# Kernel optimization log

Hardware: AMD Instinct MI355X
Metric: run time of the kernel (lower is better)

Reference implementation:

```python
import jax, jax.numpy as jnp
import numpy as np

D_MODEL = 1024
NUM_HEADS = 16
D_KEY = 64
CTX = 2048
B, T = 2, 2048


def setup_inputs() -> dict:
    key = jax.random.key(0)
    ks = jax.random.split(key, 5)
    scale_in = 1.0 / np.sqrt(D_MODEL)
    scale_out = 1.0 / np.sqrt(NUM_HEADS * D_KEY)
    return {
        "X": jax.random.normal(ks[0], (B, T, D_MODEL), dtype=jnp.float32),
        "Wqkv": jax.random.uniform(ks[1], (D_MODEL, 3 * NUM_HEADS * D_KEY), dtype=jnp.float32, minval=-scale_in, maxval=scale_in),
        "bqkv": jax.random.uniform(ks[2], (3 * NUM_HEADS * D_KEY,), dtype=jnp.float32, minval=-scale_in, maxval=scale_in),
        "Wout": jax.random.uniform(ks[3], (NUM_HEADS * D_KEY, D_MODEL), dtype=jnp.float32, minval=-scale_out, maxval=scale_out),
        "bout": jax.random.uniform(ks[4], (D_MODEL,), dtype=jnp.float32, minval=-scale_out, maxval=scale_out),
    }


def reference(X, Wqkv, bqkv, Wout, bout):
    b, t, _ = X.shape
    # project and split into q, k, v: [B,T,3,H,Dk]
    qkv = (X @ Wqkv + bqkv).reshape(b, t, 3, NUM_HEADS, D_KEY)
    q = qkv[:, :, 0].transpose(0, 2, 1, 3)  # [B,H,T,Dk]
    k = qkv[:, :, 1].transpose(0, 2, 1, 3)
    v = qkv[:, :, 2].transpose(0, 2, 1, 3)
    scores = jnp.einsum("bhqd,bhkd->bhqk", q, k) / jnp.sqrt(jnp.float32(D_KEY))
    causal = jnp.tril(jnp.ones((t, t), dtype=bool))  # [T,T]
    scores = jnp.where(causal, scores, -jnp.inf)
    attn = jax.nn.softmax(scores, axis=-1)
    out = jnp.einsum("bhqk,bhkd->bhqd", attn, v)  # [B,H,T,Dk]
    out = out.transpose(0, 2, 1, 3).reshape(b, t, NUM_HEADS * D_KEY)
    return out @ Wout + bout
```

## Files before the change

### kernel.cpp

```cpp
#include <hip/hip_runtime.h>
#include <hip/hip_bf16.h>
#include <math.h>

static constexpr int Bc = 2, Hc = 16, Tc = 2048, DKc = 64, DMc = 1024, NQKV = 3072;
#define QSCALE 0.18033688011112042f

typedef unsigned short u16;
typedef unsigned int u32;
typedef short s8v __attribute__((ext_vector_type(8)));
typedef float f32x4 __attribute__((ext_vector_type(4)));
typedef float f32x16 __attribute__((ext_vector_type(16)));
typedef int i32x4 __attribute__((ext_vector_type(4)));

#define DEVINL __device__ __forceinline__

DEVINL u16 f2b(float f) {
    union { float f; unsigned u; } v; v.f = f;
    unsigned u = v.u;
    unsigned r = (u + 0x7fffu + ((u >> 16) & 1u)) >> 16;
    return (u16)r;
}

DEVINL u32 pkbf16(float lo, float up) {
    u32 r;
    asm volatile("v_cvt_pk_bf16_f32 %0, %1, %2" : "=v"(r) : "v"(lo), "v"(up));
    return r;
}

DEVINL float vexp2(float x) {
    float r;
    asm("v_exp_f32 %0, %1" : "=v"(r) : "v"(x));
    return r;
}

DEVINL void pl32swap(u32& a, u32& b) {
    asm volatile("v_permlane32_swap_b32 %0, %1" : "+v"(a), "+v"(b));
}

DEVINL void gl_lds(const void* g, void* l) {
    __builtin_amdgcn_global_load_lds(
        (const __attribute__((address_space(1))) unsigned int*)g,
        (__attribute__((address_space(3))) unsigned int*)l, 16, 0, 0);
}

DEVINL s8v as_s8v(i32x4 x) { union { i32x4 i; s8v v; } u; u.i = x; return u.v; }

DEVINL void transw_tile(const float* __restrict__ W, u16* __restrict__ Wt,
                        int N, int K, int n0, int k0, u16 (*LT)[72], int t) {
    const int rr = t >> 4, cc = (t & 15) * 4;
    #pragma unroll
    for (int it = 0; it < 4; it++) {
        const int row = it * 16 + rr;
        float4 f = *(const float4*)&W[(size_t)(k0 + row) * N + n0 + cc];
        union { u16 u[4]; uint2 d; } o;
        o.u[0] = f2b(f.x); o.u[1] = f2b(f.y); o.u[2] = f2b(f.z); o.u[3] = f2b(f.w);
        *(uint2*)&LT[row][cc] = o.d;
    }
    __syncthreads();
    #pragma unroll
    for (int it = 0; it < 4; it++) {
        const int nrow = it * 16 + rr;
        union { u16 u[4]; uint2 d; } o;
        #pragma unroll
        for (int j = 0; j < 4; j++) o.u[j] = LT[cc + j][nrow];
        *(uint2*)&Wt[(size_t)(n0 + nrow) * K + k0 + cc] = o.d;
    }
}

__global__ __launch_bounds__(256) void prepass(
    const float* __restrict__ X, u16* __restrict__ Xb,
    const float* __restrict__ Wqkv, u16* __restrict__ Wt1,
    const float* __restrict__ Wout, u16* __restrict__ Wt2)
{
    __shared__ u16 LT[64][72];
    const int bid = blockIdx.x, t = threadIdx.x;
    if (bid < 1024) {
        const int n4 = (Bc * Tc * DMc) / 4;
        for (int i = bid * 256 + t; i < n4; i += 1024 * 256) {
            float4 f = ((const float4*)X)[i];
            union { u16 u[4]; uint2 d; } o;
            o.u[0] = f2b(f.x); o.u[1] = f2b(f.y); o.u[2] = f2b(f.z); o.u[3] = f2b(f.w);
            ((uint2*)Xb)[i] = o.d;
        }
    } else if (bid < 1024 + 768) {
        const int b2 = bid - 1024;
        transw_tile(Wqkv, Wt1, NQKV, DMc, (b2 % 48) * 64, (b2 / 48) * 64, LT, t);
    } else {
        const int b2 = bid - 1792;
        transw_tile(Wout, Wt2, DMc, DMc, (b2 % 16) * 64, (b2 / 16) * 64, LT, t);
    }
}

template <int EPI>
__global__ __launch_bounds__(512) void gemm_cv(
    const u16* __restrict__ A, const u16* __restrict__ Bt,
    const float* __restrict__ bias,
    u16* __restrict__ q_out, u16* __restrict__ k_out, u16* __restrict__ v_out,
    float* __restrict__ f_out, int M, int N, int K, int ntn)
{
    __shared__ __align__(16) u16 Al[2][128 * 32];
    __shared__ __align__(16) u16 Bl[2][128 * 32];
    const int tid = threadIdx.x, lane = tid & 63, w = tid >> 6;
    const int qd = gridDim.x >> 3;
    const int wg = (blockIdx.x & 7) * qd + (blockIdx.x >> 3);
    const int m0 = (wg / ntn) * 128, n0 = (wg % ntn) * 128;
    const int wm = w >> 2, wn = w & 3;

    f32x4 acc[4][2] = {};
    const int nt = K >> 5;

    const int srow = tid >> 2;
    const int skc  = ((tid & 3) ^ ((srow >> 1) & 3)) * 8;

#define STG(t_, s_) do {                                                       \
        const int kk_ = (t_) << 5;                                             \
        gl_lds(A + (size_t)(m0 + srow) * K + kk_ + skc,                        \
               (char*)&Al[s_][0] + w * 1024);                                  \
        gl_lds(Bt + (size_t)(n0 + srow) * K + kk_ + skc,                       \
               (char*)&Bl[s_][0] + w * 1024);                                  \
    } while (0)
#define BARX() do { __builtin_amdgcn_sched_barrier(0);                         \
        __builtin_amdgcn_s_barrier();                                          \
        __builtin_amdgcn_sched_barrier(0); } while (0)

    STG(0, 0);
    int buf = 0;
    for (int t = 0; t < nt; t++) {
        if (t + 1 < nt) {
            STG(t + 1, buf ^ 1);
            asm volatile("s_waitcnt vmcnt(2)" ::: "memory");
        } else {
            asm volatile("s_waitcnt vmcnt(0)" ::: "memory");
        }
        BARX();
        s8v af[4], bf[2];
        #pragma unroll
        for (int mi = 0; mi < 4; mi++) {
            const int row = wm * 64 + mi * 16 + (lane & 15);
            const int slot = (lane >> 4) ^ ((row >> 1) & 3);
            af[mi] = *(const s8v*)((const char*)&Al[buf][0] + row * 64 + slot * 16);
        }
        #pragma unroll
        for (int ni = 0; ni < 2; ni++) {
            const int row = wn * 32 + ni * 16 + (lane & 15);
            const int slot = (lane >> 4) ^ ((row >> 1) & 3);
            bf[ni] = *(const s8v*)((const char*)&Bl[buf][0] + row * 64 + slot * 16);
        }
        #pragma unroll
        for (int mi = 0; mi < 4; mi++)
            #pragma unroll
            for (int ni = 0; ni < 2; ni++)
                acc[mi][ni] = __builtin_amdgcn_mfma_f32_16x16x32_bf16(af[mi], bf[ni], acc[mi][ni], 0, 0, 0);
        BARX();
        buf ^= 1;
    }
#undef STG
#undef BARX

    #pragma unroll
    for (int mi = 0; mi < 4; mi++)
    #pragma unroll
    for (int ni = 0; ni < 2; ni++)
    #pragma unroll
    for (int r = 0; r < 4; r++) {
        const int row = m0 + wm * 64 + mi * 16 + (lane >> 4) * 4 + r;
        const int col = n0 + wn * 32 + ni * 16 + (lane & 15);
        const float val = acc[mi][ni][r] + bias[col];
        if constexpr (EPI == 0) {
            const int sel = col >> 10, rem = col & 1023;
            const int h = rem >> 6, d = rem & 63;
            const int b = row >> 11, tt = row & 2047;
            const size_t idx = ((size_t)(b * Hc + h) * Tc + tt) * DKc + d;
            if (sel == 0) q_out[idx] = f2b(val * QSCALE);
            else if (sel == 1) k_out[idx] = f2b(val);
            else v_out[idx] = f2b(val);
        } else {
            f_out[(size_t)row * N + col] = val;
        }
    }
}

__global__ __launch_bounds__(512) void attn_fwd(
    const u16* __restrict__ Q, const u16* __restrict__ K,
    const u16* __restrict__ V, u16* __restrict__ O)
{
    __shared__ __align__(16) char Gl[2][2][2][8192];

    const int bid = blockIdx.x;
    const int bh = bid & 31;
    const int qt = 15 - (bid >> 5);
    const int tid = threadIdx.x;
    const int g = tid >> 8;
    const int gtid = tid & 255;
    const int lane = tid & 63;
    const int ws = (tid >> 6) & 3;
    const int hi = lane >> 5, lq = lane & 31;
    const int q0w = qt * 128 + ws * 32;
    const int qg = q0w + lq;

    const u16* Qb = Q + (size_t)bh * (Tc * DKc);
    const u16* Kb = K + (size_t)bh * (Tc * DKc);
    const u16* Vb = V + (size_t)bh * (Tc * DKc);

    s8v qf[4];
    #pragma unroll
    for (int st = 0; st < 4; st++)
        qf[st] = *(const s8v*)(Qb + (size_t)qg * 64 + st * 16 + hi * 8);

    f32x16 o0 = {}, o1 = {}, lacc = {};

    const int dtw = (q0w + 31) >> 6;
    const int h = qt + 1;
    const int t0 = g * h;

    char* const Kbase = &Gl[g][0][0][0];
    char* const Vbase = &Gl[g][1][0][0];

    const int d2 = (gtid & 31) * 2, kb8 = gtid >> 5;
    const unsigned vsw0 = ((unsigned)(d2 & 7)) << 4;
    const unsigned vsw1 = ((unsigned)((d2 + 1) & 7)) << 4;
    const unsigned ksw = ((unsigned)(lq & 7)) << 4;

    u32 vx[8];

#define ISSUE_K(kt_, dst_) do {                                              \
        const char* Ktile_ = (const char*)(Kb + (size_t)(kt_) * 4096);       \
        _Pragma("unroll")                                                    \
        for (int s_ = 0; s_ < 2; s_++) {                                     \
            const int o_ = s_ * 4096 + gtid * 16;                            \
            const int rk_ = o_ >> 7;                                         \
            const int cb_ = (o_ & 127) ^ ((rk_ & 7) << 4);                   \
            gl_lds(Ktile_ + rk_ * 128 + cb_, (dst_) + s_ * 4096 + ws * 1024); \
        }                                                                    \
    } while (0)

#define LOAD_V(kt_) do {                                                     \
        const u16* Vtile_ = Vb + (size_t)(kt_) * 4096;                       \
        _Pragma("unroll")                                                    \
        for (int i_ = 0; i_ < 8; i_++)                                       \
            vx[i_] = *(const u32*)(Vtile_ + (kb8 * 8 + i_) * 64 + d2);       \
    } while (0)

#define WRITE_V(dst_) do {                                                   \
        s8v v0_, v1_;                                                        \
        _Pragma("unroll")                                                    \
        for (int i_ = 0; i_ < 8; i_++) {                                     \
            v0_[i_] = (short)(vx[i_] & 0xffff);                              \
            v1_[i_] = (short)(vx[i_] >> 16);                                 \
        }                                                                    \
        *(s8v*)((dst_) + d2 * 128 + (((unsigned)(kb8 * 16)) ^ vsw0)) = v0_;  \
        *(s8v*)((dst_) + (d2 + 1) * 128 + (((unsigned)(kb8 * 16)) ^ vsw1)) = v1_; \
    } while (0)

    ISSUE_K(t0, Kbase);
    LOAD_V(t0);
    WRITE_V(Vbase);
    __syncthreads();

    int c = 0;
    for (int i = 0; i < h; i++) {
        const int tki = t0 + i;
        const bool pf_next = (i + 1 < h);
        if (pf_next) {
            ISSUE_K(tki + 1, Kbase + (c ^ 1) * 8192);
            LOAD_V(tki + 1);
        }

        if (tki <= dtw) {
            const char* Kc = Kbase + c * 8192;
            const char* Vc = Vbase + c * 8192;
            f32x16 s0v = {}, s1v = {};
            __builtin_amdgcn_s_setprio(1);
            #pragma unroll
            for (int st = 0; st < 4; st++) {
                const unsigned cbs = (unsigned)(st * 32 + hi * 16);
                s8v kf0 = *(const s8v*)(Kc + lq * 128 + (cbs ^ ksw));
                s8v kf1 = *(const s8v*)(Kc + (32 + lq) * 128 + (cbs ^ ksw));
                s0v = __builtin_amdgcn_mfma_f32_32x32x16_bf16(kf0, qf[st], s0v, 0, 0, 0);
                s1v = __builtin_amdgcn_mfma_f32_32x32x16_bf16(kf1, qf[st], s1v, 0, 0, 0);
            }
            __builtin_amdgcn_s_setprio(0);

            if (tki == dtw) {
                #pragma unroll
                for (int r = 0; r < 16; r++) {
                    const int kg = tki * 64 + (r & 3) + 8 * (r >> 2) + 4 * hi;
                    if (kg > qg) s0v[r] = -INFINITY;
                    if (kg + 32 > qg) s1v[r] = -INFINITY;
                }
            }

            #pragma unroll
            for (int r = 0; r < 16; r++) {
                s0v[r] = vexp2(s0v[r]);
                s1v[r] = vexp2(s1v[r]);
            }
            lacc += s0v;
            lacc += s1v;

            i32x4 pf[4];
            #pragma unroll
            for (int gq = 0; gq < 2; gq++) {
                #pragma unroll
                for (int hq = 0; hq < 2; hq++) {
                    const int base = hq * 8;
                    u32 a0, a1, b0, b1;
                    if (gq == 0) {
                        a0 = pkbf16(s0v[base + 0], s0v[base + 1]);
                        a1 = pkbf16(s0v[base + 2], s0v[base + 3]);
                        b0 = pkbf16(s0v[base + 4], s0v[base + 5]);
                        b1 = pkbf16(s0v[base + 6], s0v[base + 7]);
                    } else {
                        a0 = pkbf16(s1v[base + 0], s1v[base + 1]);
                        a1 = pkbf16(s1v[base + 2], s1v[base + 3]);
                        b0 = pkbf16(s1v[base + 4], s1v[base + 5]);
                        b1 = pkbf16(s1v[base + 6], s1v[base + 7]);
                    }
                    pl32swap(a0, b0);
                    pl32swap(a1, b1);
                    pf[gq * 2 + hq][0] = (int)a0;
                    pf[gq * 2 + hq][1] = (int)a1;
                    pf[gq * 2 + hq][2] = (int)b0;
                    pf[gq * 2 + hq][3] = (int)b1;
                }
            }

            __builtin_amdgcn_s_setprio(1);
            #pragma unroll
            for (int ks = 0; ks < 4; ks++) {
                const unsigned cbv = (unsigned)(ks * 32 + hi * 16);
                s8v vf0 = *(const s8v*)(Vc + lq * 128 + (cbv ^ ksw));
                s8v vf1 = *(const s8v*)(Vc + (32 + lq) * 128 + (cbv ^ ksw));
                const s8v pa = as_s8v(pf[ks]);
                o0 = __builtin_amdgcn_mfma_f32_32x32x16_bf16(pa, vf0, o0, 0, 0, 0);
                o1 = __builtin_amdgcn_mfma_f32_32x32x16_bf16(pa, vf1, o1, 0, 0, 0);
            }
            __builtin_amdgcn_s_setprio(0);
        }

        if (pf_next) WRITE_V(Vbase + (c ^ 1) * 8192);
        __syncthreads();
        c ^= 1;
    }

    float t8[8];
    #pragma unroll
    for (int r = 0; r < 8; r++) t8[r] = lacc[r] + lacc[r + 8];
    #pragma unroll
    for (int off = 4; off >= 1; off >>= 1)
        #pragma unroll
        for (int r = 0; r < off; r++) t8[r] = t8[r] + t8[r + off];
    float ls = t8[0] + __shfl_xor(t8[0], 32);

    float* Pf = (float*)(&Gl[0][0][0][0]) + ws * 2304;
    if (g == 1) {
        float* dst = Pf + lane * 34;
        #pragma unroll
        for (int r = 0; r < 16; r++) { dst[r] = o0[r]; dst[16 + r] = o1[r]; }
        Pf[2176 + lane] = ls;
    }
    __syncthreads();
    if (g == 0) {
        const float* src = Pf + lane * 34;
        #pragma unroll
        for (int r = 0; r < 16; r++) { o0[r] += src[r]; o1[r] += src[16 + r]; }
        ls += Pf[2176 + lane];

        const float linv = 1.0f / ls;
        const int b = bh >> 4, hh = bh & 15;
        u16* Ob = O + ((size_t)b * Tc) * DMc + hh * 64;
        #pragma unroll
        for (int r = 0; r < 16; r++) {
            const int cr = (r & 3) + 8 * (r >> 2) + 4 * hi;
            const float ir = __shfl(linv, cr);
            u16* orow = Ob + (size_t)(q0w + cr) * DMc;
            orow[lq]      = f2b(o0[r] * ir);
            orow[32 + lq] = f2b(o1[r] * ir);
        }
    }
#undef ISSUE_K
#undef LOAD_V
#undef WRITE_V
}

extern "C" void kernel_launch(void* const* d_in, const int* in_sizes, int n_in,
                              void* d_out, int out_size, void* d_ws, size_t ws_size,
                              hipStream_t stream)
{
    const float* X    = (const float*)d_in[0];
    const float* Wqkv = (const float*)d_in[1];
    const float* bqkv = (const float*)d_in[2];
    const float* Wout = (const float*)d_in[3];
    const float* bout = (const float*)d_in[4];
    float* out = (float*)d_out;

    char* ws = (char*)d_ws;
    u16* Xb  = (u16*)(ws);
    u16* Ow  = (u16*)(ws);
    u16* Wt1 = (u16*)(ws + (8 << 20));
    u16* Wt2 = (u16*)(ws + (14 << 20));
    u16* Qw  = (u16*)(ws + (16 << 20));
    u16* Kw  = (u16*)(ws + (24 << 20));
    u16* Vw  = (u16*)(ws + (32 << 20));

    prepass<<<2048, 256, 0, stream>>>(X, Xb, Wqkv, Wt1, Wout, Wt2);

    gemm_cv<0><<<768, 512, 0, stream>>>(
        Xb, Wt1, bqkv, Qw, Kw, Vw, nullptr, Bc * Tc, NQKV, DMc, NQKV / 128);

    attn_fwd<<<512, 512, 0, stream>>>(Qw, Kw, Vw, Ow);

    gemm_cv<1><<<256, 512, 0, stream>>>(
        Ow, Wt2, bout, nullptr, nullptr, nullptr, out, Bc * Tc, DMc, DMc, DMc / 128);
}
```

Measured before the change: 99.39 us.

## Add intra-block split-K GEMM for QKV projection with 4-stage LDS ring

Adds a new QKV projection GEMM in which two wave groups each handle alternate 32-wide K slices of a 128x128 tile. Each group uses a 2x2 wave grid with 64x64 per-wave accumulators, and the two partial sums are reduced through LDS before the fused bias and scatter epilogue. Loads are staged through a 4-slot swizzled LDS ring with explicit vmcnt waits, double-step prefetching, and raised scheduling priority around the MFMA block. The intent is more MFMA work per LDS fragment load and better latency hiding. In exchange it uses more LDS and registers per block and adds an extra reduction step.

After: 107.7 us. 1.08x slower.

```diff
diff --git a/kernel.cpp b/kernel.cpp
--- a/kernel.cpp
+++ b/kernel.cpp
@@ -88,6 +88,121 @@
     } else {
         const int b2 = bid - 1792;
         transw_tile(Wout, Wt2, DMc, DMc, (b2 % 16) * 64, (b2 / 16) * 64, LT, t);
+    }
+}
+
+template <int EPI>
+__global__ __launch_bounds__(512, 4) void gemm_ks(
+    const u16* __restrict__ A, const u16* __restrict__ Bt,
+    const float* __restrict__ bias,
+    u16* __restrict__ q_out, u16* __restrict__ k_out, u16* __restrict__ v_out,
+    float* __restrict__ f_out, int M, int N, int K, int ntn)
+{
+    __shared__ __align__(16) char Lds[70656];
+    const int tid = threadIdx.x, lane = tid & 63, w = tid >> 6;
+    const int qd = gridDim.x >> 3;
+    const int wg = (blockIdx.x & 7) * qd + (blockIdx.x >> 3);
+    const int m0 = (wg / ntn) * 128, n0 = (wg % ntn) * 128;
+    const int g = w >> 2, sub = w & 3;
+    const int wgm = sub >> 1, wgn = sub & 1;
+
+    f32x4 acc[4][4] = {};
+    const int R = K >> 6;
+
+    const int srow = tid >> 2;
+    const int skc  = ((tid & 3) ^ ((srow >> 1) & 3)) * 8;
+
+#define STG2(j_) do {                                                          \
+        const int ta_ = 2 * (j_), tb_ = ta_ + 1;                               \
+        gl_lds(A  + (size_t)(m0 + srow) * K + ta_ * 32 + skc,                  \
+               Lds + (ta_ & 3) * 8192 + w * 1024);                             \
+        gl_lds(Bt + (size_t)(n0 + srow) * K + ta_ * 32 + skc,                  \
+               Lds + 32768 + (ta_ & 3) * 8192 + w * 1024);                     \
+        gl_lds(A  + (size_t)(m0 + srow) * K + tb_ * 32 + skc,                  \
+               Lds + (tb_ & 3) * 8192 + w * 1024);                             \
+        gl_lds(Bt + (size_t)(n0 + srow) * K + tb_ * 32 + skc,                  \
+               Lds + 32768 + (tb_ & 3) * 8192 + w * 1024);                     \
+    } while (0)
+#define BARX() do { __builtin_amdgcn_sched_barrier(0);                         \
+        __builtin_amdgcn_s_barrier();                                          \
+        __builtin_amdgcn_sched_barrier(0); } while (0)
+
+    STG2(0);
+    for (int r = 0; r < R; ++r) {
+        if (r + 1 < R) {
+            STG2(r + 1);
+            asm volatile("s_waitcnt vmcnt(4)" ::: "memory");
+        } else {
+            asm volatile("s_waitcnt vmcnt(0)" ::: "memory");
+        }
+        BARX();
+        const int sl = (2 * r + g) & 3;
+        const char* Abase = Lds + sl * 8192;
+        const char* Bbase = Lds + 32768 + sl * 8192;
+        s8v af[4], bf[4];
+        #pragma unroll
+        for (int mi = 0; mi < 4; mi++) {
+            const int row = wgm * 64 + mi * 16 + (lane & 15);
+            const int s16 = (lane >> 4) ^ ((row >> 1) & 3);
+            af[mi] = *(const s8v*)(Abase + row * 64 + s16 * 16);
+        }
+        #pragma unroll
+        for (int ni = 0; ni < 4; ni++) {
+            const int row = wgn * 64 + ni * 16 + (lane & 15);
+            const int s16 = (lane >> 4) ^ ((row >> 1) & 3);
+            bf[ni] = *(const s8v*)(Bbase + row * 64 + s16 * 16);
+        }
+        __builtin_amdgcn_s_setprio(1);
+        #pragma unroll
+        for (int mi = 0; mi < 4; mi++)
+            #pragma unroll
+            for (int ni = 0; ni < 4; ni++)
+                acc[mi][ni] = __builtin_amdgcn_mfma_f32_16x16x32_bf16(
+                    af[mi], bf[ni], acc[mi][ni], 0, 0, 0);
+        __builtin_amdgcn_s_setprio(0);
+        BARX();
+    }
+#undef STG2
+#undef BARX
+
+    if (g == 1) {
+        char* dst = Lds + sub * 17408 + lane * 272;
+        #pragma unroll
+        for (int mi = 0; mi < 4; mi++)
+            #pragma unroll
+            for (int ni = 0; ni < 4; ni++)
+                *(f32x4*)(dst + (mi * 4 + ni) * 16) = acc[mi][ni];
+    }
+    __syncthreads();
+    if (g == 0) {
+        const char* src = Lds + sub * 17408 + lane * 272;
+        #pragma unroll
+        for (int mi = 0; mi < 4; mi++)
+            #pragma unroll
+            for (int ni = 0; ni < 4; ni++)
+                acc[mi][ni] += *(const f32x4*)(src + (mi * 4 + ni) * 16);
+
+        #pragma unroll
+        for (int mi = 0; mi < 4; mi++)
+        #pragma unroll
+        for (int ni = 0; ni < 4; ni++)
+        #pragma unroll
+        for (int r = 0; r < 4; r++) {
+            const int row = m0 + wgm * 64 + mi * 16 + (lane >> 4) * 4 + r;
+            const int col = n0 + wgn * 64 + ni * 16 + (lane & 15);
+            const float val = acc[mi][ni][r] + bias[col];
+            if constexpr (EPI == 0) {
+                const int sel = col >> 10, rem = col & 1023;
+                const int h = rem >> 6, d = rem & 63;
+                const int b = row >> 11, tt = row & 2047;
+                const size_t idx = ((size_t)(b * Hc + h) * Tc + tt) * DKc + d;
+                if (sel == 0) q_out[idx] = f2b(val * QSCALE);
+                else if (sel == 1) k_out[idx] = f2b(val);
+                else v_out[idx] = f2b(val);
+            } else {
+                f_out[(size_t)row * N + col] = val;
+            }
+        }
     }
 }
 
@@ -405,7 +520,7 @@
 
     prepass<<<2048, 256, 0, stream>>>(X, Xb, Wqkv, Wt1, Wout, Wt2);
 
-    gemm_cv<0><<<768, 512, 0, stream>>>(
+    gemm_ks<0><<<768, 512, 0, stream>>>(
         Xb, Wt1, bqkv, Qw, Kw, Vw, nullptr, Bc * Tc, NQKV, DMc, NQKV / 128);
 
     attn_fwd<<<512, 512, 0, stream>>>(Qw, Kw, Vw, Ow);
```
